# Optimization experiments

Hardware: AMD Instinct MI355X
Metric: run time of the kernel (lower is better)

Reference implementation:

```python
import jax, jax.numpy as jnp
import numpy as np

EPS = 1e-8

def _phi(x):
    # elu(x) + 1
    return jax.nn.elu(x) + 1.0

def setup_inputs() -> dict:
    key = jax.random.key(0)
    k1, k2, k3, k4 = jax.random.split(key, 4)
    n, d_input, d_k = 131072, 512, 64
    X = jax.random.normal(k1, (n, d_input), dtype=jnp.float32)
    W_q = jax.random.normal(k2, (d_input, d_k), dtype=jnp.float32)
    W_k = jax.random.normal(k3, (d_input, d_k), dtype=jnp.float32)
    W_v = jax.random.normal(k4, (d_input, d_k), dtype=jnp.float32)
    return {"X": X, "W_q": W_q, "W_k": W_k, "W_v": W_v}

def reference(X, W_q, W_k, W_v):
    # Projections: [n, d_k]
    Q_phi = _phi(X @ W_q)
    K_phi = _phi(X @ W_k)
    V = X @ W_v
    # Linear-attention accumulators (associativity: K_phi^T @ V, K_phi^T @ 1)
    KV = K_phi.T @ V                      # [d_k, d_k]
    k_sum = jnp.sum(K_phi, axis=0)        # [d_k] == K_phi.T @ ones
    Z = 1.0 / (Q_phi @ k_sum[:, None] + EPS)  # [n, 1]
    out = (Q_phi @ KV) * Z                # [n, d_k]
    return out
```

## Files before the change

### kernel.cpp

```cpp
#include <hip/hip_runtime.h>
#include <hip/hip_bf16.h>

#define N_ROWS 131072
#define D_IN   512
#define DK     64

typedef short bf16x8 __attribute__((ext_vector_type(8)));
typedef float f32x4  __attribute__((ext_vector_type(4)));

__device__ __forceinline__ unsigned short f2bf(float f) {
    union { float f; unsigned u; } v; v.f = f;
    unsigned r = v.u + 0x7FFFu + ((v.u >> 16) & 1u);
    return (unsigned short)(r >> 16);
}
__device__ __forceinline__ float bf2f(unsigned short h) {
    union { unsigned u; float f; } v; v.u = ((unsigned)h) << 16;
    return v.f;
}
__device__ __forceinline__ float phi_f(float x) {
    return x > 0.f ? (x + 1.f) : __expf(x);
}

__global__ void la_prep(const float* __restrict__ Wq, const float* __restrict__ Wk,
                        const float* __restrict__ Wv, unsigned short* __restrict__ wbfT,
                        float* __restrict__ finals) {
    int idx = blockIdx.x * 1024 + threadIdx.x;
    if (idx < 4160) finals[idx] = 0.f;
    if (idx < 192 * 512) {
        int cc = idx >> 9;
        int k  = idx & 511;
        const float* W = (cc < 64) ? Wq : (cc < 128 ? Wk : Wv);
        wbfT[idx] = f2bf(W[k * DK + (cc & 63)]);
    }
}

#define XS 72
#define WSR 72
#define TS 136

__global__ __launch_bounds__(768) void la_main(
    const float* __restrict__ X, const unsigned short* __restrict__ wbfT,
    unsigned short* __restrict__ qphi, float* __restrict__ part)
{
    __shared__ __align__(16) char smem[46080];
    __shared__ float ksum_lds[64];

    unsigned short* xs  = (unsigned short*)smem;
    unsigned short* wsm = (unsigned short*)(smem + 18432);
    unsigned short* kT  = (unsigned short*)smem;
    unsigned short* vT  = (unsigned short*)(smem + 17408);

    const int tid = threadIdx.x;
    const int w   = tid >> 6;
    const int l   = tid & 63;
    const int c   = l & 15;
    const int g   = l >> 4;
    const int sec = w % 3;
    const int r   = w / 3;
    const long rowBase = (long)blockIdx.x * 128;

    if (tid < 64) ksum_lds[tid] = 0.f;

    f32x4 acc[2][4];
#pragma unroll
    for (int m = 0; m < 2; ++m)
#pragma unroll
        for (int f = 0; f < 4; ++f) acc[m][f] = (f32x4){0.f, 0.f, 0.f, 0.f};

    for (int kb = 0; kb < D_IN / 64; ++kb) {
        const int k0 = kb * 64;
        for (int i = tid; i < 2048; i += 768) {
            const int rl = i >> 4, c4 = i & 15;
            const float4 xv = *(const float4*)(X + (rowBase + rl) * D_IN + k0 + (c4 << 2));
            const unsigned u0 = (unsigned)f2bf(xv.x) | ((unsigned)f2bf(xv.y) << 16);
            const unsigned u1 = (unsigned)f2bf(xv.z) | ((unsigned)f2bf(xv.w) << 16);
            *(uint2*)(xs + rl * XS + (c4 << 2)) = make_uint2(u0, u1);
        }
        for (int i = tid; i < 1536; i += 768) {
            const int cc = i >> 3, ch = i & 7;
            *(float4*)(wsm + cc * WSR + (ch << 3)) =
                *(const float4*)(wbfT + cc * D_IN + k0 + (ch << 3));
        }
        __syncthreads();
#pragma unroll
        for (int ks = 0; ks < 2; ++ks) {
            const int ko = ks * 32 + g * 8;
            bf16x8 a[2], b[4];
#pragma unroll
            for (int m = 0; m < 2; ++m)
                a[m] = *(const bf16x8*)(xs + (r * 32 + m * 16 + c) * XS + ko);
#pragma unroll
            for (int f = 0; f < 4; ++f)
                b[f] = *(const bf16x8*)(wsm + (sec * 64 + f * 16 + c) * WSR + ko);
#pragma unroll
            for (int m = 0; m < 2; ++m)
#pragma unroll
                for (int f = 0; f < 4; ++f)
                    acc[m][f] = __builtin_amdgcn_mfma_f32_16x16x32_bf16(a[m], b[f], acc[m][f], 0, 0, 0);
        }
        __syncthreads();
    }

    if (sec == 0) {
#pragma unroll
        for (int m = 0; m < 2; ++m)
#pragma unroll
            for (int f = 0; f < 4; ++f)
#pragma unroll
                for (int reg = 0; reg < 4; ++reg) {
                    const long row = rowBase + r * 32 + m * 16 + g * 4 + reg;
                    qphi[row * DK + f * 16 + c] = f2bf(phi_f(acc[m][f][reg]));
                }
    } else if (sec == 1) {
        float s[4] = {0.f, 0.f, 0.f, 0.f};
#pragma unroll
        for (int m = 0; m < 2; ++m)
#pragma unroll
            for (int f = 0; f < 4; ++f) {
                float p0 = phi_f(acc[m][f][0]), p1 = phi_f(acc[m][f][1]);
                float p2 = phi_f(acc[m][f][2]), p3 = phi_f(acc[m][f][3]);
                s[f] += p0 + p1 + p2 + p3;
                const int col = f * 16 + c;
                const int row0 = r * 32 + m * 16 + g * 4;
                *(unsigned*)(kT + col * TS + row0)     = (unsigned)f2bf(p0) | ((unsigned)f2bf(p1) << 16);
                *(unsigned*)(kT + col * TS + row0 + 2) = (unsigned)f2bf(p2) | ((unsigned)f2bf(p3) << 16);
            }
#pragma unroll
        for (int f = 0; f < 4; ++f) {
            s[f] += __shfl_xor(s[f], 16);
            s[f] += __shfl_xor(s[f], 32);
        }
        if (l < 16)
#pragma unroll
            for (int f = 0; f < 4; ++f) atomicAdd(&ksum_lds[f * 16 + c], s[f]);
    } else {
#pragma unroll
        for (int m = 0; m < 2; ++m)
#pragma unroll
            for (int f = 0; f < 4; ++f) {
                const int col = f * 16 + c;
                const int row0 = r * 32 + m * 16 + g * 4;
                *(unsigned*)(vT + col * TS + row0) =
                    (unsigned)f2bf(acc[m][f][0]) | ((unsigned)f2bf(acc[m][f][1]) << 16);
                *(unsigned*)(vT + col * TS + row0 + 2) =
                    (unsigned)f2bf(acc[m][f][2]) | ((unsigned)f2bf(acc[m][f][3]) << 16);
            }
    }
    __syncthreads();

    float* partBlk = part + (long)blockIdx.x * 4160;
    if (w < 4) {
        f32x4 kv[4];
#pragma unroll
        for (int f = 0; f < 4; ++f) kv[f] = (f32x4){0.f, 0.f, 0.f, 0.f};
#pragma unroll
        for (int ks = 0; ks < 4; ++ks) {
            const int ko = ks * 32 + g * 8;
            bf16x8 a = *(const bf16x8*)(kT + (w * 16 + c) * TS + ko);
#pragma unroll
            for (int f = 0; f < 4; ++f) {
                bf16x8 b = *(const bf16x8*)(vT + (f * 16 + c) * TS + ko);
                kv[f] = __builtin_amdgcn_mfma_f32_16x16x32_bf16(a, b, kv[f], 0, 0, 0);
            }
        }
#pragma unroll
        for (int f = 0; f < 4; ++f)
#pragma unroll
            for (int reg = 0; reg < 4; ++reg)
                partBlk[(w * 16 + g * 4 + reg) * 64 + f * 16 + c] = kv[f][reg];
    }
    if (tid < 64) partBlk[4096 + tid] = ksum_lds[tid];
}

__global__ void la_reduce(const float* __restrict__ part, float* __restrict__ finals) {
    const int e  = (blockIdx.x % 65) * 64 + threadIdx.x;
    const int bs = blockIdx.x / 65;
    if (e < 4160) {
        float s = 0.f;
        const float* p = part + (long)bs * 128 * 4160 + e;
        for (int b = 0; b < 128; ++b) s += p[(long)b * 4160];
        atomicAdd(&finals[e], s);
    }
}

__global__ __launch_bounds__(256) void la_out(
    const unsigned short* __restrict__ qphi, const float* __restrict__ finals,
    float* __restrict__ out)
{
    __shared__ __align__(16) unsigned short kvT[64 * 72];
    __shared__ float ks_l[64];
    __shared__ float z_l[4][32];

    const int tid = threadIdx.x;
    const int w = tid >> 6, l = tid & 63, c = l & 15, g = l >> 4;

    const int e0 = tid << 4;
    const int kk = e0 >> 6, j0 = e0 & 63;
#pragma unroll
    for (int q = 0; q < 16; ++q) kvT[(j0 + q) * 72 + kk] = f2bf(finals[e0 + q]);
    if (tid < 64) ks_l[tid] = finals[4096 + tid];
    __syncthreads();

    const long rowBase = (long)blockIdx.x * 128 + w * 32;

    bf16x8 a[2][2];
#pragma unroll
    for (int m = 0; m < 2; ++m)
#pragma unroll
        for (int ks = 0; ks < 2; ++ks)
            a[m][ks] = *(const bf16x8*)(qphi + (rowBase + m * 16 + c) * DK + ks * 32 + g * 8);

#pragma unroll
    for (int m = 0; m < 2; ++m) {
        float den = 0.f;
#pragma unroll
        for (int ks = 0; ks < 2; ++ks)
#pragma unroll
            for (int i = 0; i < 8; ++i)
                den += bf2f((unsigned short)a[m][ks][i]) * ks_l[ks * 32 + g * 8 + i];
        den += __shfl_xor(den, 16);
        den += __shfl_xor(den, 32);
        if (l < 16) z_l[w][m * 16 + c] = 1.f / (den + 1e-8f);
    }

    f32x4 acc[2][4];
#pragma unroll
    for (int m = 0; m < 2; ++m)
#pragma unroll
        for (int f = 0; f < 4; ++f) acc[m][f] = (f32x4){0.f, 0.f, 0.f, 0.f};
#pragma unroll
    for (int ks = 0; ks < 2; ++ks)
#pragma unroll
        for (int f = 0; f < 4; ++f) {
            bf16x8 b = *(const bf16x8*)(kvT + (f * 16 + c) * 72 + ks * 32 + g * 8);
#pragma unroll
            for (int m = 0; m < 2; ++m)
                acc[m][f] = __builtin_amdgcn_mfma_f32_16x16x32_bf16(a[m][ks], b, acc[m][f], 0, 0, 0);
        }

#pragma unroll
    for (int m = 0; m < 2; ++m)
#pragma unroll
        for (int reg = 0; reg < 4; ++reg) {
            const int row16 = g * 4 + reg;
            const float z = z_l[w][m * 16 + row16];
#pragma unroll
            for (int f = 0; f < 4; ++f)
                out[(rowBase + m * 16 + row16) * DK + f * 16 + c] = acc[m][f][reg] * z;
        }
}

extern "C" void kernel_launch(void* const* d_in, const int* in_sizes, int n_in,
                              void* d_out, int out_size, void* d_ws, size_t ws_size,
                              hipStream_t stream) {
    const float* X  = (const float*)d_in[0];
    const float* Wq = (const float*)d_in[1];
    const float* Wk = (const float*)d_in[2];
    const float* Wv = (const float*)d_in[3];
    float* out = (float*)d_out;

    char* ws = (char*)d_ws;
    unsigned short* qphi  = (unsigned short*)ws;
    unsigned short* wbfT  = (unsigned short*)(ws + 16777216);
    float*          part  = (float*)(ws + 16777216 + 196608);
    float*          fin   = (float*)(ws + 16777216 + 196608 + 17039360);

    la_prep  <<<96,   1024, 0, stream>>>(Wq, Wk, Wv, wbfT, fin);
    la_main  <<<1024,  768, 0, stream>>>(X, wbfT, qphi, part);
    la_reduce<<<520,    64, 0, stream>>>(part, fin);
    la_out   <<<1024,  256, 0, stream>>>(qphi, fin, out);
}
```

Baseline: 421.0 us.

## Double-buffer LDS tiles and prefetch next K-block into registers

The projection GEMM loop now uses two LDS buffers for X and weight tiles. The next K-block of global data is loaded into registers while the MFMAs for the current block run, and one of the two barriers per iteration is dropped. The aim is to hide global memory latency behind compute. In exchange, LDS use doubles to about 92KB per block and register pressure rises, which may lower occupancy at 768 threads.

```diff
diff --git a/kernel.cpp b/kernel.cpp
--- a/kernel.cpp
+++ b/kernel.cpp
@@ -42,13 +42,15 @@
     const float* __restrict__ X, const unsigned short* __restrict__ wbfT,
     unsigned short* __restrict__ qphi, float* __restrict__ part)
 {
-    __shared__ __align__(16) char smem[46080];
+    __shared__ __align__(16) char smem[92160];
     __shared__ float ksum_lds[64];
 
-    unsigned short* xs  = (unsigned short*)smem;
-    unsigned short* wsm = (unsigned short*)(smem + 18432);
-    unsigned short* kT  = (unsigned short*)smem;
-    unsigned short* vT  = (unsigned short*)(smem + 17408);
+    unsigned short* xsb[2] = { (unsigned short*)smem,
+                               (unsigned short*)(smem + 18432) };
+    unsigned short* wsb[2] = { (unsigned short*)(smem + 36864),
+                               (unsigned short*)(smem + 64512) };
+    unsigned short* kT = (unsigned short*)smem;
+    unsigned short* vT = (unsigned short*)(smem + 17408);
 
     const int tid = threadIdx.x;
     const int w   = tid >> 6;
@@ -67,21 +69,61 @@
 #pragma unroll
         for (int f = 0; f < 4; ++f) acc[m][f] = (f32x4){0.f, 0.f, 0.f, 0.f};
 
-    for (int kb = 0; kb < D_IN / 64; ++kb) {
-        const int k0 = kb * 64;
-        for (int i = tid; i < 2048; i += 768) {
-            const int rl = i >> 4, c4 = i & 15;
-            const float4 xv = *(const float4*)(X + (rowBase + rl) * D_IN + k0 + (c4 << 2));
-            const unsigned u0 = (unsigned)f2bf(xv.x) | ((unsigned)f2bf(xv.y) << 16);
-            const unsigned u1 = (unsigned)f2bf(xv.z) | ((unsigned)f2bf(xv.w) << 16);
-            *(uint2*)(xs + rl * XS + (c4 << 2)) = make_uint2(u0, u1);
-        }
-        for (int i = tid; i < 1536; i += 768) {
-            const int cc = i >> 3, ch = i & 7;
-            *(float4*)(wsm + cc * WSR + (ch << 3)) =
-                *(const float4*)(wbfT + cc * D_IN + k0 + (ch << 3));
-        }
+    float4 xr0, xr1, xr2, xr3;
+    float4 wr0, wr1;
+
+    const int xsl = tid;
+    const int xrl0 = (xsl) >> 4,          xc0 = (xsl) & 15;
+    const int xrl1 = (xsl + 512) >> 4,    xc1 = (xsl + 512) & 15;
+    const int xrl2 = (xsl + 1024) >> 4,   xc2 = (xsl + 1024) & 15;
+    const int xrl3 = (xsl + 1536) >> 4,   xc3 = (xsl + 1536) & 15;
+    const int wcc0 = tid >> 3,           wch0 = tid & 7;
+    const int wcc1 = (tid + 768) >> 3,   wch1 = (tid + 768) & 7;
+
+    {
+        const int k0 = 0;
+        if (tid < 512) {
+            xr0 = *(const float4*)(X + (rowBase + xrl0) * D_IN + k0 + (xc0 << 2));
+            xr1 = *(const float4*)(X + (rowBase + xrl1) * D_IN + k0 + (xc1 << 2));
+            xr2 = *(const float4*)(X + (rowBase + xrl2) * D_IN + k0 + (xc2 << 2));
+            xr3 = *(const float4*)(X + (rowBase + xrl3) * D_IN + k0 + (xc3 << 2));
+        }
+        wr0 = *(const float4*)(wbfT + wcc0 * D_IN + k0 + (wch0 << 3));
+        wr1 = *(const float4*)(wbfT + wcc1 * D_IN + k0 + (wch1 << 3));
+    }
+
+#pragma unroll
+    for (int kb = 0; kb < 8; ++kb) {
+        unsigned short* xs  = xsb[kb & 1];
+        unsigned short* wsm = wsb[kb & 1];
+        if (tid < 512) {
+            {   const unsigned u0 = (unsigned)f2bf(xr0.x) | ((unsigned)f2bf(xr0.y) << 16);
+                const unsigned u1 = (unsigned)f2bf(xr0.z) | ((unsigned)f2bf(xr0.w) << 16);
+                *(uint2*)(xs + xrl0 * XS + (xc0 << 2)) = make_uint2(u0, u1); }
+            {   const unsigned u0 = (unsigned)f2bf(xr1.x) | ((unsigned)f2bf(xr1.y) << 16);
+                const unsigned u1 = (unsigned)f2bf(xr1.z) | ((unsigned)f2bf(xr1.w) << 16);
+                *(uint2*)(xs + xrl1 * XS + (xc1 << 2)) = make_uint2(u0, u1); }
+            {   const unsigned u0 = (unsigned)f2bf(xr2.x) | ((unsigned)f2bf(xr2.y) << 16);
+                const unsigned u1 = (unsigned)f2bf(xr2.z) | ((unsigned)f2bf(xr2.w) << 16);
+                *(uint2*)(xs + xrl2 * XS + (xc2 << 2)) = make_uint2(u0, u1); }
+            {   const unsigned u0 = (unsigned)f2bf(xr3.x) | ((unsigned)f2bf(xr3.y) << 16);
+                const unsigned u1 = (unsigned)f2bf(xr3.z) | ((unsigned)f2bf(xr3.w) << 16);
+                *(uint2*)(xs + xrl3 * XS + (xc3 << 2)) = make_uint2(u0, u1); }
+        }
+        *(float4*)(wsm + wcc0 * WSR + (wch0 << 3)) = wr0;
+        *(float4*)(wsm + wcc1 * WSR + (wch1 << 3)) = wr1;
         __syncthreads();
+        if (kb < 7) {
+            const int k0 = (kb + 1) * 64;
+            if (tid < 512) {
+                xr0 = *(const float4*)(X + (rowBase + xrl0) * D_IN + k0 + (xc0 << 2));
+                xr1 = *(const float4*)(X + (rowBase + xrl1) * D_IN + k0 + (xc1 << 2));
+                xr2 = *(const float4*)(X + (rowBase + xrl2) * D_IN + k0 + (xc2 << 2));
+                xr3 = *(const float4*)(X + (rowBase + xrl3) * D_IN + k0 + (xc3 << 2));
+            }
+            wr0 = *(const float4*)(wbfT + wcc0 * D_IN + k0 + (wch0 << 3));
+            wr1 = *(const float4*)(wbfT + wcc1 * D_IN + k0 + (wch1 << 3));
+        }
 #pragma unroll
         for (int ks = 0; ks < 2; ++ks) {
             const int ko = ks * 32 + g * 8;
@@ -98,8 +140,8 @@
                 for (int f = 0; f < 4; ++f)
                     acc[m][f] = __builtin_amdgcn_mfma_f32_16x16x32_bf16(a[m], b[f], acc[m][f], 0, 0, 0);
         }
-        __syncthreads();
-    }
+    }
+    __syncthreads();
 
     if (sec == 0) {
 #pragma unroll
```

Result: faster. 396.9 us (-5.7%).
